# Performance work log

Hardware: AMD Instinct MI355X
Metric: run time of the kernel (lower is better)

## Reference

```python
import jax, jax.numpy as jnp
import numpy as np
from jax import lax

T, D, H, O = 16384, 257, 512, 257


def setup_inputs() -> dict:
    key = jax.random.key(0)
    ks = jax.random.split(key, 7)
    s = 1.0 / np.sqrt(H)  # PyTorch LSTM/Linear uniform init scale
    u = lambda k, shp: jax.random.uniform(k, shp, jnp.float32, -s, s)
    return {
        "stft": jax.random.normal(ks[0], (T, D), jnp.float32),
        "W_ih": u(ks[1], (4 * H, D)),
        "W_hh": u(ks[2], (4 * H, H)),
        "b_ih": u(ks[3], (4 * H,)),
        "b_hh": u(ks[4], (4 * H,)),
        "W_out": u(ks[5], (O, H)),
        "b_out": u(ks[6], (O,)),
    }


def reference(stft, W_ih, W_hh, b_ih, b_hh, W_out, b_out):
    # Batch size is 1 (stft.view(T, 1, -1)), so we scan over [T, D] directly.
    # Precompute input-to-gate GEMM for all timesteps: [T, 4H]
    x_gates = stft @ W_ih.T + (b_ih + b_hh)

    def step(carry, xg):
        h, c = carry  # [H], [H]
        g = xg + h @ W_hh.T  # [4H], PyTorch gate order: i, f, g, o
        i, f, gg, o = jnp.split(g, 4)
        i = jax.nn.sigmoid(i)
        f = jax.nn.sigmoid(f)
        gg = jnp.tanh(gg)
        o = jax.nn.sigmoid(o)
        c = f * c + i * gg
        h = o * jnp.tanh(c)
        return (h, c), h

    h0 = jnp.zeros((H,), stft.dtype)  # init_hidden(): zeros
    c0 = jnp.zeros((H,), stft.dtype)
    _, hs = lax.scan(step, (h0, c0), x_gates)  # hs: [T, H]

    out_space = hs @ W_out.T + b_out  # [T, O]
    return jax.nn.log_softmax(out_space, axis=1)
```

## Files before the change

kernel.cpp:

```cpp
#include <hip/hip_runtime.h>
#include <cmath>

#define T_STEPS 16384
#define D_IN    257
#define H_DIM   512
#define O_DIM   257
#define G4      2048

typedef unsigned long long u64;

#define WS_XG_OFF     8192
#define WS_HS_OFF     (8192 + (size_t)T_STEPS * G4 * 4)

__device__ inline float fast_sigmoid(float x) {
    return 1.f / (1.f + __expf(-x));
}
__device__ inline float fast_tanh(float x) {
    float ax = fminf(fabsf(x), 15.f);
    float e  = __expf(2.f * ax);
    float t  = (e - 1.f) / (e + 1.f);
    return copysignf(t, x);
}
__device__ inline float dot4(float4 a, float4 b) {
    return a.x * b.x + a.y * b.y + a.z * b.z + a.w * b.w;
}

#define PIN4(v) asm volatile("" : "+v"(v.x), "+v"(v.y), "+v"(v.z), "+v"(v.w))

__global__ __launch_bounds__(256) void xgate_gemm(
    const float* __restrict__ stft, const float* __restrict__ W_ih,
    const float* __restrict__ b_ih, const float* __restrict__ b_hh,
    float* __restrict__ xg)
{
    const int tid = threadIdx.x;
    const int tx = tid & 15, ty = tid >> 4;
    const int j0 = blockIdx.x * 64;
    const int t0 = blockIdx.y * 64;

    __shared__ float s_a[64][17];
    __shared__ float s_b[64][17];

    float acc[4][4] = {};

    for (int k0 = 0; k0 < D_IN; k0 += 16) {
        #pragma unroll
        for (int l = 0; l < 4; ++l) {
            int idx = tid + l * 256;
            int r  = idx >> 4;
            int kk = idx & 15;
            int k  = k0 + kk;
            s_a[r][kk] = (k < D_IN) ? stft[(size_t)(t0 + r) * D_IN + k] : 0.f;
            s_b[r][kk] = (k < D_IN) ? W_ih[(size_t)(j0 + r) * D_IN + k] : 0.f;
        }
        __syncthreads();
        #pragma unroll
        for (int kk = 0; kk < 16; ++kk) {
            float a[4], b[4];
            #pragma unroll
            for (int r = 0; r < 4; ++r) a[r] = s_a[ty * 4 + r][kk];
            #pragma unroll
            for (int c = 0; c < 4; ++c) b[c] = s_b[tx * 4 + c][kk];
            #pragma unroll
            for (int r = 0; r < 4; ++r)
                #pragma unroll
                for (int c = 0; c < 4; ++c)
                    acc[r][c] += a[r] * b[c];
        }
        __syncthreads();
    }

    float bias[4];
    #pragma unroll
    for (int c = 0; c < 4; ++c) {
        int j = j0 + tx * 4 + c;
        bias[c] = b_ih[j] + b_hh[j];
    }
    #pragma unroll
    for (int r = 0; r < 4; ++r) {
        int t = t0 + ty * 4 + r;
        #pragma unroll
        for (int c = 0; c < 4; ++c) {
            xg[(size_t)t * G4 + j0 + tx * 4 + c] = acc[r][c] + bias[c];
        }
    }
}

__global__ __launch_bounds__(512, 1) void lstm_seq(
    const float* __restrict__ W_hh, const float* __restrict__ xg,
    float* __restrict__ hs, u64* __restrict__ msg)
{
    const int tid  = threadIdx.x;
    const int g    = blockIdx.x;
    const int w    = tid >> 6;
    const int lane = tid & 63;
    const int j    = lane >> 2;
    const int c    = lane & 3;
    const int colb = w * 64 + c * 16;

    const float* wbase = W_hh + (size_t)(g * 16 + j) * H_DIM + colb;
    const size_t gstride = (size_t)H_DIM * H_DIM;
    float4 wA0, wA1, wA2, wA3, wB0, wB1, wB2, wB3;
    float4 wC0, wC1, wC2, wC3, wD0, wD1, wD2, wD3;
    {
        const float4* p0 = (const float4*)(wbase);
        const float4* p1 = (const float4*)(wbase + gstride);
        const float4* p2 = (const float4*)(wbase + 2 * gstride);
        const float4* p3 = (const float4*)(wbase + 3 * gstride);
        wA0 = p0[0]; wA1 = p0[1]; wA2 = p0[2]; wA3 = p0[3];
        wB0 = p1[0]; wB1 = p1[1]; wB2 = p1[2]; wB3 = p1[3];
        wC0 = p2[0]; wC1 = p2[1]; wC2 = p2[2]; wC3 = p2[3];
        wD0 = p3[0]; wD1 = p3[1]; wD2 = p3[2]; wD3 = p3[3];
    }
    PIN4(wA0); PIN4(wA1); PIN4(wA2); PIN4(wA3);
    PIN4(wB0); PIN4(wB1); PIN4(wB2); PIN4(wB3);
    PIN4(wC0); PIN4(wC1); PIN4(wC2); PIN4(wC3);
    PIN4(wD0); PIN4(wD1); PIN4(wD2); PIN4(wD3);

    __shared__ float s_h[512];
    __shared__ float s_part[2][512];

    u64* slot0 = msg;
    u64* slot1 = msg + 512;

    float c_state = 0.f;
    const int t_j = lane & 15;

    for (int t = 0; t < T_STEPS; ++t) {
        const unsigned tagt = (unsigned)t;
        const int buf = t & 1;

        float xv = 0.f;
        if (w == 0)
            xv = __builtin_nontemporal_load(
                xg + (size_t)t * G4 + (lane >> 4) * H_DIM + g * 16 + t_j);

        u64* rp = (buf ? slot1 : slot0) + tid;
        u64 u;
        for (;;) {
            u = __hip_atomic_load(rp, __ATOMIC_RELAXED, __HIP_MEMORY_SCOPE_AGENT);
            if ((unsigned)(u >> 32) == tagt) break;
        }

        s_h[tid] = __uint_as_float((unsigned)u);

        const float4* hv = (const float4*)(s_h + colb);
        float4 h0 = hv[0], h1 = hv[1], h2 = hv[2], h3 = hv[3];

        float p0 = dot4(wA0, h0) + dot4(wA1, h1) + dot4(wA2, h2) + dot4(wA3, h3);
        float p1 = dot4(wB0, h0) + dot4(wB1, h1) + dot4(wB2, h2) + dot4(wB3, h3);
        float p2 = dot4(wC0, h0) + dot4(wC1, h1) + dot4(wC2, h2) + dot4(wC3, h3);
        float p3 = dot4(wD0, h0) + dot4(wD1, h1) + dot4(wD2, h2) + dot4(wD3, h3);

        const bool lo2 = (c < 2);
        float a0 = (lo2 ? p0 : p2) + __shfl_xor(lo2 ? p2 : p0, 2, 64);
        float a1 = (lo2 ? p1 : p3) + __shfl_xor(lo2 ? p3 : p1, 2, 64);
        const bool ev = ((c & 1) == 0);
        float fin = (ev ? a0 : a1) + __shfl_xor(ev ? a1 : a0, 1, 64);

        s_part[buf][w * 64 + c * 16 + j] = fin;

        asm volatile("s_waitcnt lgkmcnt(0)\n\ts_barrier" ::: "memory");

        if (w == 0) {
            const float* pp = &s_part[buf][0];
            float sum = xv;
            #pragma unroll
            for (int k = 0; k < 8; ++k) sum += pp[k * 64 + lane];

            float gi = __shfl(sum, t_j + 0,  64);
            float gf = __shfl(sum, t_j + 16, 64);
            float gg = __shfl(sum, t_j + 32, 64);
            float go = __shfl(sum, t_j + 48, 64);

            float iv = fast_sigmoid(gi);
            float fv = fast_sigmoid(gf);
            float ov = fast_sigmoid(go);
            float gv = fast_tanh(gg);
            c_state = fv * c_state + iv * gv;
            float hn = ov * fast_tanh(c_state);

            if (lane < 16) {
                __builtin_nontemporal_store(hn, hs + (size_t)t * H_DIM + g * 16 + lane);
                u64 m = ((u64)(tagt + 1) << 32) | (u64)__float_as_uint(hn);
                u64* wp = (((t + 1) & 1) ? slot1 : slot0) + (g * 16 + lane);
                __hip_atomic_store(wp, m, __ATOMIC_RELAXED, __HIP_MEMORY_SCOPE_AGENT);
            }
        }
    }
}

__global__ __launch_bounds__(256) void out_softmax(
    const float* __restrict__ hs, const float* __restrict__ W_out,
    const float* __restrict__ b_out, float* __restrict__ out)
{
    const int tid = threadIdx.x;
    const int t0  = blockIdx.x * 16;

    __shared__ float s_w[257 * 33];
    __shared__ float s_hs[16 * 33];
    __shared__ float s_o[16 * 257];
    __shared__ float s_red[8];

    float acc[16] = {};
    float acc256 = 0.f;

    for (int k0 = 0; k0 < H_DIM; k0 += 32) {
        for (int idx = tid; idx < 257 * 32; idx += 256) {
            int row = idx >> 5, col = idx & 31;
            s_w[row * 33 + col] = W_out[(size_t)row * H_DIM + k0 + col];
        }
        for (int idx = tid; idx < 16 * 32; idx += 256) {
            int row = idx >> 5, col = idx & 31;
            s_hs[row * 33 + col] = hs[(size_t)(t0 + row) * H_DIM + k0 + col];
        }
        __syncthreads();
        #pragma unroll
        for (int kk = 0; kk < 32; ++kk) {
            float w = s_w[tid * 33 + kk];
            #pragma unroll
            for (int r = 0; r < 16; ++r)
                acc[r] += s_hs[r * 33 + kk] * w;
        }
        if (tid < 16) {
            #pragma unroll
            for (int kk = 0; kk < 32; ++kk)
                acc256 += s_w[256 * 33 + kk] * s_hs[tid * 33 + kk];
        }
        __syncthreads();
    }

    float bias_c = b_out[tid];
    #pragma unroll
    for (int r = 0; r < 16; ++r) s_o[r * 257 + tid] = acc[r] + bias_c;
    if (tid < 16) s_o[tid * 257 + 256] = acc256 + b_out[256];
    __syncthreads();

    const int lane = tid & 63, wid = tid >> 6;
    for (int r = 0; r < 16; ++r) {
        float v  = s_o[r * 257 + tid];
        float vx = (tid == 0) ? s_o[r * 257 + 256] : -INFINITY;
        float m = fmaxf(v, vx);
        #pragma unroll
        for (int off = 32; off > 0; off >>= 1) m = fmaxf(m, __shfl_xor(m, off, 64));
        if (lane == 0) s_red[wid] = m;
        __syncthreads();
        m = fmaxf(fmaxf(s_red[0], s_red[1]), fmaxf(s_red[2], s_red[3]));
        float e = expf(v - m) + ((tid == 0) ? expf(vx - m) : 0.f);
        #pragma unroll
        for (int off = 32; off > 0; off >>= 1) e += __shfl_xor(e, off, 64);
        if (lane == 0) s_red[4 + wid] = e;
        __syncthreads();
        float s = s_red[4] + s_red[5] + s_red[6] + s_red[7];
        float lg = logf(s) + m;
        out[(size_t)(t0 + r) * O_DIM + tid] = v - lg;
        if (tid == 0) out[(size_t)(t0 + r) * O_DIM + 256] = vx - lg;
    }
}

extern "C" void kernel_launch(void* const* d_in, const int* in_sizes, int n_in,
                              void* d_out, int out_size, void* d_ws, size_t ws_size,
                              hipStream_t stream) {
    (void)in_sizes; (void)n_in; (void)out_size; (void)ws_size;

    const float* stft  = (const float*)d_in[0];
    const float* W_ih  = (const float*)d_in[1];
    const float* W_hh  = (const float*)d_in[2];
    const float* b_ih  = (const float*)d_in[3];
    const float* b_hh  = (const float*)d_in[4];
    const float* W_out = (const float*)d_in[5];
    const float* b_out = (const float*)d_in[6];
    float* out = (float*)d_out;

    char* ws = (char*)d_ws;
    u64* msg  = (u64*)ws;
    float* xg = (float*)(ws + WS_XG_OFF);
    float* hs = (float*)(ws + WS_HS_OFF);

    (void)hipMemsetAsync(ws, 0, 8192, stream);

    xgate_gemm<<<dim3(G4 / 64, T_STEPS / 64), 256, 0, stream>>>(
        stft, W_ih, b_ih, b_hh, xg);
    lstm_seq<<<32, 512, 0, stream>>>(W_hh, xg, hs, msg);
    out_softmax<<<T_STEPS / 16, 256, 0, stream>>>(hs, W_out, b_out, out);
}
```

Baseline: 24.69 ms.

## Publish pre-activation gates instead of hidden state, compute activations redundantly in every block

Each block now publishes its summed gate pre-activations (with the next step's input gate term already added) to a 2048-entry tagged message buffer, in place of the hidden-state values. Every block reads all four gate pre-activations for every hidden unit and computes the cell update redundantly. This takes the activation math and the intra-wave shuffles off the critical path between the barrier and the cross-block publish, and the next step's xg load is prefetched. The cost is four times the polled atomic traffic per step, plus redundant transcendental work in all 32 blocks.

```diff
diff --git a/kernel.cpp b/kernel.cpp
--- a/kernel.cpp
+++ b/kernel.cpp
@@ -9,8 +9,8 @@
 
 typedef unsigned long long u64;
 
-#define WS_XG_OFF     8192
-#define WS_HS_OFF     (8192 + (size_t)T_STEPS * G4 * 4)
+#define WS_XG_OFF     32768
+#define WS_HS_OFF     (32768 + (size_t)T_STEPS * G4 * 4)
 
 __device__ inline float fast_sigmoid(float x) {
     return 1.f / (1.f + __expf(-x));
@@ -96,6 +96,8 @@
     const int j    = lane >> 2;
     const int c    = lane & 3;
     const int colb = w * 64 + c * 16;
+
+    const int prow = (lane >> 4) * H_DIM + g * 16 + (lane & 15);
 
     const float* wbase = W_hh + (size_t)(g * 16 + j) * H_DIM + colb;
     const size_t gstride = (size_t)H_DIM * H_DIM;
@@ -111,80 +113,85 @@
         wC0 = p2[0]; wC1 = p2[1]; wC2 = p2[2]; wC3 = p2[3];
         wD0 = p3[0]; wD1 = p3[1]; wD2 = p3[2]; wD3 = p3[3];
     }
-    PIN4(wA0); PIN4(wA1); PIN4(wA2); PIN4(wA3);
-    PIN4(wB0); PIN4(wB1); PIN4(wB2); PIN4(wB3);
-    PIN4(wC0); PIN4(wC1); PIN4(wC2); PIN4(wC3);
-    PIN4(wD0); PIN4(wD1); PIN4(wD2); PIN4(wD3);
 
     __shared__ float s_h[512];
     __shared__ float s_part[2][512];
 
-    u64* slot0 = msg;
-    u64* slot1 = msg + 512;
-
     float c_state = 0.f;
-    const int t_j = lane & 15;
 
     for (int t = 0; t < T_STEPS; ++t) {
+        const int buf = t & 1;
         const unsigned tagt = (unsigned)t;
-        const int buf = t & 1;
-
-        float xv = 0.f;
-        if (w == 0)
-            xv = __builtin_nontemporal_load(
-                xg + (size_t)t * G4 + (lane >> 4) * H_DIM + g * 16 + t_j);
-
-        u64* rp = (buf ? slot1 : slot0) + tid;
-        u64 u;
-        for (;;) {
-            u = __hip_atomic_load(rp, __ATOMIC_RELAXED, __HIP_MEMORY_SCOPE_AGENT);
-            if ((unsigned)(u >> 32) == tagt) break;
-        }
-
-        s_h[tid] = __uint_as_float((unsigned)u);
+
+        float xnext = 0.f;
+        if (w == 0 && t + 1 < T_STEPS)
+            xnext = __builtin_nontemporal_load(xg + (size_t)(t + 1) * G4 + prow);
+
+        float s0, s1, s2, s3;
+        if (t == 0) {
+            s0 = xg[tid];
+            s1 = xg[512 + tid];
+            s2 = xg[1024 + tid];
+            s3 = xg[1536 + tid];
+        } else {
+            u64* bp = msg + (size_t)buf * 2048;
+            u64 a0, a1, a2, a3;
+            for (;;) {
+                a0 = __hip_atomic_load(bp + tid,        __ATOMIC_RELAXED, __HIP_MEMORY_SCOPE_AGENT);
+                a1 = __hip_atomic_load(bp + 512 + tid,  __ATOMIC_RELAXED, __HIP_MEMORY_SCOPE_AGENT);
+                a2 = __hip_atomic_load(bp + 1024 + tid, __ATOMIC_RELAXED, __HIP_MEMORY_SCOPE_AGENT);
+                a3 = __hip_atomic_load(bp + 1536 + tid, __ATOMIC_RELAXED, __HIP_MEMORY_SCOPE_AGENT);
+                if ((unsigned)(a0 >> 32) == tagt && (unsigned)(a1 >> 32) == tagt &&
+                    (unsigned)(a2 >> 32) == tagt && (unsigned)(a3 >> 32) == tagt) break;
+            }
+            s0 = __uint_as_float((unsigned)a0);
+            s1 = __uint_as_float((unsigned)a1);
+            s2 = __uint_as_float((unsigned)a2);
+            s3 = __uint_as_float((unsigned)a3);
+        }
+
+        float iv = fast_sigmoid(s0);
+        float fv = fast_sigmoid(s1);
+        float gv = fast_tanh(s2);
+        float ov = fast_sigmoid(s3);
+        c_state = fv * c_state + iv * gv;
+        float hn = ov * fast_tanh(c_state);
+
+        if ((tid >> 4) == g)
+            __builtin_nontemporal_store(hn, hs + (size_t)t * H_DIM + tid);
+
+        s_h[tid] = hn;
+
+        PIN4(wA0); PIN4(wA1); PIN4(wA2); PIN4(wA3);
+        PIN4(wB0); PIN4(wB1); PIN4(wB2); PIN4(wB3);
+        PIN4(wC0); PIN4(wC1); PIN4(wC2); PIN4(wC3);
+        PIN4(wD0); PIN4(wD1); PIN4(wD2); PIN4(wD3);
 
         const float4* hv = (const float4*)(s_h + colb);
         float4 h0 = hv[0], h1 = hv[1], h2 = hv[2], h3 = hv[3];
-
         float p0 = dot4(wA0, h0) + dot4(wA1, h1) + dot4(wA2, h2) + dot4(wA3, h3);
         float p1 = dot4(wB0, h0) + dot4(wB1, h1) + dot4(wB2, h2) + dot4(wB3, h3);
         float p2 = dot4(wC0, h0) + dot4(wC1, h1) + dot4(wC2, h2) + dot4(wC3, h3);
         float p3 = dot4(wD0, h0) + dot4(wD1, h1) + dot4(wD2, h2) + dot4(wD3, h3);
 
         const bool lo2 = (c < 2);
-        float a0 = (lo2 ? p0 : p2) + __shfl_xor(lo2 ? p2 : p0, 2, 64);
-        float a1 = (lo2 ? p1 : p3) + __shfl_xor(lo2 ? p3 : p1, 2, 64);
+        float a0f = (lo2 ? p0 : p2) + __shfl_xor(lo2 ? p2 : p0, 2, 64);
+        float a1f = (lo2 ? p1 : p3) + __shfl_xor(lo2 ? p3 : p1, 2, 64);
         const bool ev = ((c & 1) == 0);
-        float fin = (ev ? a0 : a1) + __shfl_xor(ev ? a1 : a0, 1, 64);
+        float fin = (ev ? a0f : a1f) + __shfl_xor(ev ? a1f : a0f, 1, 64);
 
         s_part[buf][w * 64 + c * 16 + j] = fin;
 
         asm volatile("s_waitcnt lgkmcnt(0)\n\ts_barrier" ::: "memory");
 
-        if (w == 0) {
+        if (w == 0 && t + 1 < T_STEPS) {
             const float* pp = &s_part[buf][0];
-            float sum = xv;
+            float sum = xnext;
             #pragma unroll
             for (int k = 0; k < 8; ++k) sum += pp[k * 64 + lane];
-
-            float gi = __shfl(sum, t_j + 0,  64);
-            float gf = __shfl(sum, t_j + 16, 64);
-            float gg = __shfl(sum, t_j + 32, 64);
-            float go = __shfl(sum, t_j + 48, 64);
-
-            float iv = fast_sigmoid(gi);
-            float fv = fast_sigmoid(gf);
-            float ov = fast_sigmoid(go);
-            float gv = fast_tanh(gg);
-            c_state = fv * c_state + iv * gv;
-            float hn = ov * fast_tanh(c_state);
-
-            if (lane < 16) {
-                __builtin_nontemporal_store(hn, hs + (size_t)t * H_DIM + g * 16 + lane);
-                u64 m = ((u64)(tagt + 1) << 32) | (u64)__float_as_uint(hn);
-                u64* wp = (((t + 1) & 1) ? slot1 : slot0) + (g * 16 + lane);
-                __hip_atomic_store(wp, m, __ATOMIC_RELAXED, __HIP_MEMORY_SCOPE_AGENT);
-            }
+            u64 m = ((u64)(tagt + 1) << 32) | (u64)__float_as_uint(sum);
+            __hip_atomic_store(msg + (size_t)((t + 1) & 1) * 2048 + prow, m,
+                               __ATOMIC_RELAXED, __HIP_MEMORY_SCOPE_AGENT);
         }
     }
 }
@@ -276,7 +283,7 @@
     float* xg = (float*)(ws + WS_XG_OFF);
     float* hs = (float*)(ws + WS_HS_OFF);
 
-    (void)hipMemsetAsync(ws, 0, 8192, stream);
+    (void)hipMemsetAsync(ws, 0, 32768, stream);
 
     xgate_gemm<<<dim3(G4 / 64, T_STEPS / 64), 256, 0, stream>>>(
         stft, W_ih, b_ih, b_hh, xg);
```

New measurement: 32.00 ms. 29.6% more time.
